# Optimization experiments

Measured on AMD Instinct MI355X. Metric: run time of the kernel, lower is better.

## Reference

```python
import jax, jax.numpy as jnp
import numpy as np

N = 4096          # total ensemble boxes per frame
M = 20            # MAX_MERGE_NUMS
H = 16            # MergeNet hidden_c
COND_THRES = 0.2
IOU_THRES = 0.3


def setup_inputs() -> dict:
    key = jax.random.key(0)
    ks = jax.random.split(key, 6)
    u = jax.random.uniform(ks[0], (N, 9), dtype=jnp.float32)
    # realistic lidar boxes: centers in a ~140x80x8m range, dims in [0.5, 4.5), heading in [-pi, pi)
    centers = (u[:, 0:3] - 0.5) * jnp.array([140.0, 80.0, 8.0], jnp.float32)
    dims = u[:, 3:6] * 4.0 + 0.5
    heading = (u[:, 6:7] - 0.5) * (2.0 * np.pi)
    extra = u[:, 7:9]  # extra box attrs (cols 7:9), untouched by merge
    pred_boxes = jnp.concatenate([centers, dims, heading, extra], axis=-1)
    pred_scores = jax.random.uniform(ks[1], (N,), dtype=jnp.float32)
    pred_labels = jax.random.randint(ks[2], (N,), 0, 3)
    w1 = (jax.random.normal(ks[3], (M, H), jnp.float32) / np.sqrt(M)).astype(jnp.float32)
    b1 = jnp.zeros((H,), jnp.float32)
    w2 = (jax.random.normal(ks[4], (H, H), jnp.float32) / np.sqrt(H)).astype(jnp.float32)
    b2 = jnp.zeros((H,), jnp.float32)
    w3 = (jax.random.normal(ks[5], (H, 1), jnp.float32) / np.sqrt(H)).astype(jnp.float32)
    b3 = jnp.zeros((1,), jnp.float32)
    return dict(pred_boxes=pred_boxes, pred_scores=pred_scores, pred_labels=pred_labels,
                w1=w1, b1=b1, w2=w2, b2=b2, w3=w3, b3=b3)


def _bev_aligned(b):
    # boxes3d_lidar_to_aligned_bev_boxes: swap dx/dy when |limit_period(heading)| >= pi/4
    ang = b[..., 6] - jnp.floor(b[..., 6] / np.pi + 0.5) * np.pi
    swap = jnp.abs(ang) >= (np.pi / 4)
    dx = jnp.where(swap, b[..., 4], b[..., 3])
    dy = jnp.where(swap, b[..., 3], b[..., 4])
    return jnp.stack([b[..., 0] - dx / 2, b[..., 1] - dy / 2,
                      b[..., 0] + dx / 2, b[..., 1] + dy / 2], axis=-1)


def _iou_one_many(a, b):
    # axis-aligned BEV IoU of one box a[4] vs many b[N,4]
    xmin = jnp.maximum(a[0], b[:, 0]); ymin = jnp.maximum(a[1], b[:, 1])
    xmax = jnp.minimum(a[2], b[:, 2]); ymax = jnp.minimum(a[3], b[:, 3])
    inter = jnp.maximum(xmax - xmin, 0.0) * jnp.maximum(ymax - ymin, 0.0)
    area_a = (a[2] - a[0]) * (a[3] - a[1])
    area_b = (b[:, 2] - b[:, 0]) * (b[:, 3] - b[:, 1])
    return inter / jnp.maximum(area_a + area_b - inter, 1e-6)


def _nms_merge(pred_boxes, pred_scores, pred_labels, w1, b1, w2, b2, w3, b3):
    valid = pred_scores > COND_THRES
    sort_key = jnp.where(valid, pred_scores, -jnp.inf)
    order = jnp.argsort(-sort_key)                 # descending by score; invalid sink
    boxes9 = pred_boxes[order]
    labels = pred_labels[order]
    scores = pred_scores[order]
    suppressed0 = ~valid[order]
    boxes7 = boxes9[:, :7]
    bev0 = _bev_aligned(boxes7)                    # merged boxes get suppressed, so bev is static

    def mergenet(ob):                              # ob: [M, 7] -> merged box [7]
        x = ob.T                                   # [7, M] (k is the feature axis)
        h = jax.nn.relu(x @ w1 + b1)
        h = jax.nn.relu(h @ w2 + b2)
        return (h @ w3 + b3)[:, 0]

    def step(suppressed, i):
        active = ~suppressed[i]
        same = (labels == labels[i]) & (~suppressed)
        iou = _iou_one_many(bev0[i], bev0)         # [N]
        over = (iou > IOU_THRES) & same            # includes self (iou=1)
        count = jnp.sum(over)
        rank = jnp.cumsum(over) - 1                # slot of each overlap, in score order
        tgt = jnp.where(over & (rank < M), rank, M)
        ob = jnp.zeros((M, 7), boxes7.dtype).at[tgt].set(boxes7, mode='drop')
        bi = boxes7[i]
        new_box = jnp.where(count > 1, mergenet(ob), bi)
        new_box = new_box.at[3:6].set(jnp.maximum(new_box[3:6], 1e-5))
        out_box = jnp.where(active, new_box, bi)
        return suppressed | (over & active), (out_box, active)

    _, (merged7, keep) = jax.lax.scan(step, suppressed0, jnp.arange(N))
    out_boxes = jnp.concatenate([merged7, boxes9[:, 7:9]], axis=-1)   # [N, 9]
    return out_boxes, scores, labels, keep


def reference(pred_boxes, pred_scores, pred_labels, w1, b1, w2, b2, w3, b3):
    # Returns fixed-shape (boxes9, scores, labels, keep_mask); rows with keep=False
    # correspond to boxes that torch's dynamic version would have removed.
    return _nms_merge(pred_boxes, pred_scores, pred_labels, w1, b1, w2, b2, w3, b3)
```

## Files before the change

kernel.cpp:

```cpp
#include <hip/hip_runtime.h>
#include <cstdint>

typedef unsigned long long u64;
typedef unsigned int u32;

#define NB 4096
#define NW 64
#define MM 20
#define HH 16
#define COND_THRES 0.2f
#define IOU_THRES 0.3f
#define PI_F  3.14159265358979323846f
#define PI4_F 0.78539816339744830962f

#define WS_KEPT    0
#define WS_MASK    32768
#define WS_BOX9S   (WS_MASK + NB*NW*8)
#define WS_BEVS    (WS_BOX9S + NB*9*4)
#define WS_SCORES  (WS_BEVS + NB*16)
#define WS_LABELS  (WS_SCORES + NB*4)
#define WS_NBRW    (WS_LABELS + NB*4)
#define WS_SUPSTEP (WS_NBRW + NB*8)

__device__ __forceinline__ u64 sort_key(float s, int i) {
  u32 sb = (s > COND_THRES) ? __float_as_uint(s) : 0u;
  return ((u64)(sb ^ 0xFFFFFFFFu) << 12) | (u64)i;
}

__global__ void __launch_bounds__(256) k_prep(const float* __restrict__ scores,
                                              const float* __restrict__ boxes9,
                                              const int* __restrict__ labels,
                                              float* __restrict__ box9s, float4* __restrict__ bevs,
                                              float* __restrict__ scoress, int* __restrict__ labelss,
                                              u64* __restrict__ nbrw) {
  #pragma clang fp contract(off)
  __shared__ u64 keys[NB];
  __shared__ u32 part[16][16];
  int tid = threadIdx.x;
  for (int k = tid; k < NB; k += 256) keys[k] = sort_key(scores[k], k);
  __syncthreads();
  int bl = tid & 15;
  int ch = tid >> 4;
  u64 ki = keys[blockIdx.x * 16 + bl];
  int c = 0;
  #pragma unroll 16
  for (int t = 0; t < 256; ++t) c += (keys[(ch << 8) + t] < ki) ? 1 : 0;
  part[bl][ch] = (u32)c;
  __syncthreads();
  if (tid < 16) {
    int i = blockIdx.x * 16 + tid;
    int r = 0;
    #pragma unroll
    for (int q = 0; q < 16; ++q) r += (int)part[tid][q];
    nbrw[i] = 0;
    float b[9];
    #pragma unroll
    for (int f = 0; f < 9; ++f) b[f] = boxes9[i * 9 + f];
    #pragma unroll
    for (int f = 0; f < 9; ++f) box9s[r * 9 + f] = b[f];
    float ang = b[6] - floorf(b[6] / PI_F + 0.5f) * PI_F;
    bool sw = fabsf(ang) >= PI4_F;
    float dx = sw ? b[4] : b[3];
    float dy = sw ? b[3] : b[4];
    bevs[r] = make_float4(b[0] - dx * 0.5f, b[1] - dy * 0.5f,
                          b[0] + dx * 0.5f, b[1] + dy * 0.5f);
    scoress[r] = scores[i];
    labelss[r] = labels[i];
  }
}

__global__ void __launch_bounds__(64) k_mask(const float4* __restrict__ bevs,
                                             const int* __restrict__ labelss,
                                             const float* __restrict__ scoress,
                                             u64* __restrict__ mask,
                                             u64* __restrict__ nbrw) {
  #pragma clang fp contract(off)
  __shared__ float4 bj[64];
  __shared__ int lj[64];
  __shared__ u64 tw[64];
  int t = threadIdx.x;
  int b = blockIdx.x;
  int it = (int)((sqrtf(8.0f * (float)b + 1.0f) - 1.0f) * 0.5f);
  while ((it + 1) * (it + 2) / 2 <= b) ++it;
  while (it * (it + 1) / 2 > b) --it;
  int jt = b - it * (it + 1) / 2;
  int j = jt * 64 + t;
  bj[t] = bevs[j];
  lj[t] = labelss[j];
  u64 vj = __ballot(scoress[j] > COND_THRES);
  int i = it * 64 + t;
  float4 a = bevs[i];
  int la = labelss[i];
  float area_a = (a.z - a.x) * (a.w - a.y);
  __syncthreads();
  u64 w = 0;
  #pragma unroll 8
  for (int kk = 0; kk < 64; ++kk) {
    float4 bb = bj[kk];
    float xmin = fmaxf(a.x, bb.x), ymin = fmaxf(a.y, bb.y);
    float xmax = fminf(a.z, bb.z), ymax = fminf(a.w, bb.w);
    float inter = fmaxf(xmax - xmin, 0.0f) * fmaxf(ymax - ymin, 0.0f);
    float area_b = (bb.z - bb.x) * (bb.w - bb.y);
    float iou = inter / fmaxf(area_a + area_b - inter, 1e-6f);
    if ((iou > IOU_THRES) && (la == lj[kk])) w |= (1ull << kk);
  }
  mask[(u64)i * NW + jt] = w;
  {
    u64 below = (jt < it) ? ~0ull : ((1ull << t) - 1ull);
    if (w & vj & below) atomicOr(&nbrw[i], 1ull << jt);
  }
  if (jt < it) {
    tw[t] = w;
    __syncthreads();
    u64 wT = 0;
    #pragma unroll 8
    for (int k = 0; k < 64; ++k) wT |= ((tw[k] >> t) & 1ull) << k;
    mask[(u64)j * NW + it] = wT;
  }
}

__global__ void __launch_bounds__(1024) k_nms(const u64* __restrict__ mask,
                                              const u64* __restrict__ nbrw,
                                              const float* __restrict__ scoress,
                                              int* __restrict__ supstep) {
  __shared__ u64 decided[64], kept[64];
  __shared__ int wavePending[16];
  __shared__ int anyPending;
  int tid = threadIdx.x;
  int lane = tid & 63;
  int waveId = tid >> 6;
  u64 dcache[4], kcache[4];
  bool validB[4];
  #pragma unroll
  for (int s = 0; s < 4; ++s) {
    int i = tid + (s << 10);
    bool v = scoress[i] > COND_THRES;
    validB[s] = v;
    u64 vw = __ballot(v);
    dcache[s] = ~vw;
    kcache[s] = 0;
    if (lane == 0) {
      int wi = waveId + (s << 4);
      decided[wi] = ~vw;
      kept[wi] = 0;
    }
  }
  u64 cw0[4], cw1[4];
  u32 meta[4];
  #pragma unroll
  for (int s = 0; s < 4; ++s) {
    int i = tid + (s << 10);
    int wi = i >> 6;
    u64 bit = 1ull << (i & 63);
    u64 t = nbrw[i];
    int n = 0; u32 ovf = 0;
    u64 c0 = 0, c1 = 0; u32 i0 = 0, i1 = 0;
    while (t) {
      int w = __builtin_ctzll(t);
      t &= t - 1;
      u64 below = (w < wi) ? ~0ull : (bit - 1ull);
      u64 m = mask[(u64)i * NW + w] & below;
      if (n == 0)      { c0 = m; i0 = (u32)w; }
      else if (n == 1) { c1 = m; i1 = (u32)w; }
      else ovf = 1;
      ++n;
    }
    cw0[s] = c0; cw1[s] = c1;
    meta[s] = i0 | (i1 << 6) | ((u32)(n > 2 ? 2 : n) << 12) | (ovf << 14);
  }
  __syncthreads();
  while (true) {
    bool pend = false;
    #pragma unroll
    for (int s = 0; s < 4; ++s) {
      bool mine_und = !((dcache[s] >> lane) & 1ull);
      bool dec = false, keepme = false;
      if (mine_und) {
        bool hasU = false, hasK = false;
        u32 mt = meta[s];
        if (!(mt & (1u << 14))) {
          int n = (mt >> 12) & 3;
          if (n >= 1) {
            int w = mt & 63;
            u64 dw = decided[w], kw = kept[w];
            hasU = (cw0[s] & ~dw) != 0ull;
            hasK = (cw0[s] & kw) != 0ull;
          }
          if (n >= 2) {
            int w = (mt >> 6) & 63;
            u64 dw = decided[w], kw = kept[w];
            hasU = hasU || ((cw1[s] & ~dw) != 0ull);
            hasK = hasK || ((cw1[s] & kw) != 0ull);
          }
        } else {
          int i = tid + (s << 10);
          int wi = i >> 6;
          u64 bit = 1ull << (i & 63);
          u64 t = nbrw[i];
          while (t) {
            int w = __builtin_ctzll(t);
            t &= t - 1;
            u64 below = (w < wi) ? ~0ull : (bit - 1ull);
            u64 m = mask[(u64)i * NW + w] & below;
            hasU = hasU || ((m & ~decided[w]) != 0ull);
            hasK = hasK || ((m & kept[w]) != 0ull);
          }
        }
        dec = !hasU;
        keepme = !hasK;
      }
      u64 b_nd = __ballot(dec);
      u64 b_nk = __ballot(dec && keepme);
      dcache[s] |= b_nd;
      kcache[s] |= b_nk;
      pend |= (mine_und && !dec);
    }
    u64 pw = __ballot(pend);
    if (lane == 0) wavePending[waveId] = (pw != 0ull) ? 1 : 0;
    __syncthreads();
    if (lane == 0) {
      #pragma unroll
      for (int s = 0; s < 4; ++s) {
        int wi = waveId + (s << 4);
        decided[wi] = dcache[s];
        kept[wi] = kcache[s];
      }
    }
    if (tid == 0) {
      int any = 0;
      #pragma unroll
      for (int w = 0; w < 16; ++w) any |= wavePending[w];
      anyPending = any;
    }
    __syncthreads();
    if (!anyPending) break;
  }
  #pragma unroll
  for (int s = 0; s < 4; ++s) {
    int j = tid + (s << 10);
    int res;
    if (!validB[s]) {
      res = -1;
    } else {
      int wj = j >> 6;
      u64 bitbelow = (1ull << (j & 63)) - 1ull;
      res = j;
      u64 t = nbrw[j];
      while (t) {
        int w = __builtin_ctzll(t);
        t &= t - 1;
        u64 m = mask[(u64)j * NW + w] & kept[w];
        if (w == wj) m &= bitbelow;
        if (m) { res = (w << 6) + __builtin_ctzll(m); break; }
      }
    }
    supstep[j] = res;
  }
}

__global__ void __launch_bounds__(64) k_merge(
    const u64* __restrict__ mask, const int* __restrict__ supstep,
    const float* __restrict__ box9s, const float* __restrict__ scoress,
    const int* __restrict__ labelss,
    const float* __restrict__ w1, const float* __restrict__ b1,
    const float* __restrict__ w2, const float* __restrict__ b2,
    const float* __restrict__ w3, const float* __restrict__ b3,
    float* __restrict__ out) {
  #pragma clang fp contract(off)
  __shared__ int candList[MM];
  __shared__ float ob[MM][7];
  __shared__ float h1[7][HH];
  __shared__ float h2[7][HH];
  __shared__ float res[7];
  int i = blockIdx.x;
  int t = threadIdx.x;
  bool active = (supstep[i] == i);
  u64 wq = 0;
  int cnt = 0;
  if (active) {
    u64 w = mask[(u64)i * NW + t];
    while (w) {
      int b = __builtin_ctzll(w);
      w &= w - 1;
      int j = (t << 6) | b;
      if (supstep[j] >= i) { wq |= (1ull << b); cnt++; }
    }
  }
  int incl = cnt;
  #pragma unroll
  for (int off = 1; off < 64; off <<= 1) {
    int v = __shfl_up(incl, off);
    if (t >= off) incl += v;
  }
  int excl = incl - cnt;
  int count = __shfl(incl, 63);
  bool merged = active && (count > 1);
  if (merged && wq) {
    int pos = excl;
    u64 ww = wq;
    while (ww && pos < MM) {
      int b = __builtin_ctzll(ww);
      ww &= ww - 1;
      candList[pos++] = (t << 6) | b;
    }
  }
  __syncthreads();
  if (merged) {
    int nc = count < MM ? count : MM;
    if (t < MM) {
      if (t < nc) {
        int j = candList[t];
        #pragma unroll
        for (int f = 0; f < 7; ++f) ob[t][f] = box9s[j * 9 + f];
      } else {
        #pragma unroll
        for (int f = 0; f < 7; ++f) ob[t][f] = 0.0f;
      }
    }
    __syncthreads();
    for (int o = t; o < 7 * HH; o += 64) {
      int f = o >> 4, hh = o & 15;
      float acc = b1[hh];
      #pragma unroll
      for (int m = 0; m < MM; ++m) acc += ob[m][f] * w1[m * HH + hh];
      h1[f][hh] = fmaxf(acc, 0.0f);
    }
    __syncthreads();
    for (int o = t; o < 7 * HH; o += 64) {
      int f = o >> 4, oo = o & 15;
      float acc = b2[oo];
      #pragma unroll
      for (int k = 0; k < HH; ++k) acc += h1[f][k] * w2[k * HH + oo];
      h2[f][oo] = fmaxf(acc, 0.0f);
    }
    __syncthreads();
    if (t < 7) {
      float acc = b3[0];
      #pragma unroll
      for (int k = 0; k < HH; ++k) acc += h2[t][k] * w3[k];
      if (t >= 3 && t < 6) acc = fmaxf(acc, 1e-5f);
      res[t] = acc;
    }
    __syncthreads();
  }
  if (t < 9) {
    float v = box9s[i * 9 + t];
    if (merged && t < 7) v = res[t];
    out[i * 9 + t] = v;
  }
  if (t == 0) {
    out[NB * 9 + i]          = scoress[i];
    out[NB * 9 + NB + i]     = (float)labelss[i];
    out[NB * 9 + 2 * NB + i] = active ? 1.0f : 0.0f;
  }
}

extern "C" void kernel_launch(void* const* d_in, const int* in_sizes, int n_in,
                              void* d_out, int out_size, void* d_ws, size_t ws_size,
                              hipStream_t stream) {
  const float* boxes9 = (const float*)d_in[0];
  const float* scores = (const float*)d_in[1];
  const int*   labels = (const int*)d_in[2];
  const float* w1 = (const float*)d_in[3];
  const float* b1 = (const float*)d_in[4];
  const float* w2 = (const float*)d_in[5];
  const float* b2 = (const float*)d_in[6];
  const float* w3 = (const float*)d_in[7];
  const float* b3 = (const float*)d_in[8];
  char* ws = (char*)d_ws;
  u64*    mask    = (u64*)(ws + WS_MASK);
  float*  box9s   = (float*)(ws + WS_BOX9S);
  float4* bevs    = (float4*)(ws + WS_BEVS);
  float*  scoress = (float*)(ws + WS_SCORES);
  int*    labelss = (int*)(ws + WS_LABELS);
  u64*    nbrw    = (u64*)(ws + WS_NBRW);
  int*    supstep = (int*)(ws + WS_SUPSTEP);
  float*  out     = (float*)d_out;

  hipLaunchKernelGGL(k_prep,  dim3(256),  dim3(256),  0, stream,
                     scores, boxes9, labels, box9s, bevs, scoress, labelss, nbrw);
  hipLaunchKernelGGL(k_mask,  dim3(2080), dim3(64),   0, stream,
                     bevs, labelss, scoress, mask, nbrw);
  hipLaunchKernelGGL(k_nms,   dim3(1),    dim3(1024), 0, stream,
                     mask, nbrw, scoress, supstep);
  hipLaunchKernelGGL(k_merge, dim3(NB),   dim3(64),   0, stream,
                     mask, supstep, box9s, scoress, labelss,
                     w1, b1, w2, b2, w3, b3, out);
}
```

Measured before the change: 112.8 us.

## Resolve NMS segments sequentially with single-barrier iterations and reuse cached mask words

The fixed-point NMS loop now resolves each of the four 1024-box segments in index order, each in its own loop, instead of iterating all segments together until the whole block converges. Each iteration uses one barrier instead of two: lane 0 updates the shared decided/kept words directly, and every thread reads the pending flags itself. The final suppressor lookup reuses the per-thread cached mask words and falls back to reading global memory only on overflow. The risks are that the per-segment iteration counts now add up rather than overlap, and that `wavePending` can be overwritten by a fast wave while a slower wave is still reading it.

```diff
diff --git a/kernel.cpp b/kernel.cpp
--- a/kernel.cpp
+++ b/kernel.cpp
@@ -125,11 +125,9 @@
                                               int* __restrict__ supstep) {
   __shared__ u64 decided[64], kept[64];
   __shared__ int wavePending[16];
-  __shared__ int anyPending;
   int tid = threadIdx.x;
   int lane = tid & 63;
   int waveId = tid >> 6;
-  u64 dcache[4], kcache[4];
   bool validB[4];
   #pragma unroll
   for (int s = 0; s < 4; ++s) {
@@ -137,12 +135,9 @@
     bool v = scoress[i] > COND_THRES;
     validB[s] = v;
     u64 vw = __ballot(v);
-    dcache[s] = ~vw;
-    kcache[s] = 0;
     if (lane == 0) {
-      int wi = waveId + (s << 4);
-      decided[wi] = ~vw;
-      kept[wi] = 0;
+      decided[waveId + (s << 4)] = ~vw;
+      kept[waveId + (s << 4)] = 0;
     }
   }
   u64 cw0[4], cw1[4];
@@ -169,15 +164,16 @@
     meta[s] = i0 | (i1 << 6) | ((u32)(n > 2 ? 2 : n) << 12) | (ovf << 14);
   }
   __syncthreads();
-  while (true) {
-    bool pend = false;
-    #pragma unroll
-    for (int s = 0; s < 4; ++s) {
-      bool mine_und = !((dcache[s] >> lane) & 1ull);
+  for (int s = 0; s < 4; ++s) {
+    const int i = tid + (s << 10);
+    const int wi = waveId + (s << 4);
+    const u64 bit = 1ull << (i & 63);
+    const u32 mt = meta[s];
+    bool und = validB[s];
+    while (true) {
       bool dec = false, keepme = false;
-      if (mine_und) {
+      if (und) {
         bool hasU = false, hasK = false;
-        u32 mt = meta[s];
         if (!(mt & (1u << 14))) {
           int n = (mt >> 12) & 3;
           if (n >= 1) {
@@ -193,9 +189,6 @@
             hasK = hasK || ((cw1[s] & kw) != 0ull);
           }
         } else {
-          int i = tid + (s << 10);
-          int wi = i >> 6;
-          u64 bit = 1ull << (i & 63);
           u64 t = nbrw[i];
           while (t) {
             int w = __builtin_ctzll(t);
@@ -211,29 +204,20 @@
       }
       u64 b_nd = __ballot(dec);
       u64 b_nk = __ballot(dec && keepme);
-      dcache[s] |= b_nd;
-      kcache[s] |= b_nk;
-      pend |= (mine_und && !dec);
-    }
-    u64 pw = __ballot(pend);
-    if (lane == 0) wavePending[waveId] = (pw != 0ull) ? 1 : 0;
-    __syncthreads();
-    if (lane == 0) {
-      #pragma unroll
-      for (int s = 0; s < 4; ++s) {
-        int wi = waveId + (s << 4);
-        decided[wi] = dcache[s];
-        kept[wi] = kcache[s];
+      bool pend = und && !dec;
+      u64 pw = __ballot(pend);
+      if (lane == 0) {
+        decided[wi] |= b_nd;
+        kept[wi] |= b_nk;
+        wavePending[waveId] = (pw != 0ull) ? 1 : 0;
       }
-    }
-    if (tid == 0) {
+      und = pend;
+      __syncthreads();
       int any = 0;
       #pragma unroll
       for (int w = 0; w < 16; ++w) any |= wavePending[w];
-      anyPending = any;
-    }
-    __syncthreads();
-    if (!anyPending) break;
+      if (!any) break;
+    }
   }
   #pragma unroll
   for (int s = 0; s < 4; ++s) {
@@ -242,16 +226,32 @@
     if (!validB[s]) {
       res = -1;
     } else {
-      int wj = j >> 6;
-      u64 bitbelow = (1ull << (j & 63)) - 1ull;
       res = j;
-      u64 t = nbrw[j];
-      while (t) {
-        int w = __builtin_ctzll(t);
-        t &= t - 1;
-        u64 m = mask[(u64)j * NW + w] & kept[w];
-        if (w == wj) m &= bitbelow;
-        if (m) { res = (w << 6) + __builtin_ctzll(m); break; }
+      u32 mt = meta[s];
+      if (!(mt & (1u << 14))) {
+        int n = (mt >> 12) & 3;
+        if (n >= 1) {
+          int w0 = mt & 63;
+          u64 m0 = cw0[s] & kept[w0];
+          if (m0) {
+            res = (w0 << 6) + __builtin_ctzll(m0);
+          } else if (n >= 2) {
+            int w1 = (mt >> 6) & 63;
+            u64 m1 = cw1[s] & kept[w1];
+            if (m1) res = (w1 << 6) + __builtin_ctzll(m1);
+          }
+        }
+      } else {
+        int wj = j >> 6;
+        u64 bitbelow = (1ull << (j & 63)) - 1ull;
+        u64 t = nbrw[j];
+        while (t) {
+          int w = __builtin_ctzll(t);
+          t &= t - 1;
+          u64 m = mask[(u64)j * NW + w] & kept[w];
+          if (w == wj) m &= bitbelow;
+          if (m) { res = (w << 6) + __builtin_ctzll(m); break; }
+        }
       }
     }
     supstep[j] = res;
```

New measurement: 111.9 us (median of 3 runs). About the same (-0.9%).
